# Kernel optimization log

Hardware: AMD Instinct MI355X
Metric: run time of the kernel (lower is better)

## Reference

```python
import jax, jax.numpy as jnp
import numpy as np

B, D, G, F, A = 262144, 128, 8, 80, 18  # batch, obs dim, n_games, n_features, max_actions


def setup_inputs() -> dict:
    key = jax.random.key(0)
    ks = jax.random.split(key, 10)
    s1 = 1.0 / np.sqrt(D)
    s2 = 1.0 / np.sqrt(F)
    state = jax.random.normal(ks[0], (B, D), dtype=jnp.float32)
    idx = jnp.sort(jax.random.randint(ks[1], (B,), 0, G, dtype=jnp.int32))
    W1 = jax.random.normal(ks[2], (G, F, D), dtype=jnp.float32) * s1
    b1 = jax.random.normal(ks[3], (G, F), dtype=jnp.float32) * s1
    W2 = jax.random.normal(ks[4], (F, F), dtype=jnp.float32) * s2
    b2 = jax.random.normal(ks[5], (F,), dtype=jnp.float32) * s2
    W3 = jax.random.normal(ks[6], (F, F), dtype=jnp.float32) * s2
    b3 = jax.random.normal(ks[7], (F,), dtype=jnp.float32) * s2
    W4 = jax.random.normal(ks[8], (G, A, F), dtype=jnp.float32) * s2
    b4 = jax.random.normal(ks[9], (G, A), dtype=jnp.float32) * s2
    return {"state": state, "idx": idx, "W1": W1, "b1": b1, "W2": W2, "b2": b2,
            "W3": W3, "b3": b3, "W4": W4, "b4": b4}


def reference(state, idx, W1, b1, W2, b2, W3, b3, W4, b4):
    state = state.astype(jnp.float32)
    n_games = W1.shape[0]
    # Routed first layer: each sample goes through its game's Linear(D->F).
    # Loop is over the small fixed set of games; batch dim stays vectorized.
    h1 = jnp.zeros((state.shape[0], W1.shape[1]), dtype=state.dtype)
    for g in range(n_games):
        hg = state @ W1[g].T + b1[g]  # [B, F]
        h1 = h1 + jnp.where((idx == g)[:, None], hg, jnp.zeros((), state.dtype))
    h1 = jax.nn.relu(h1)
    # Shared MLP (features == 'relu')
    h = jax.nn.relu(h1 @ W2.T + b2)
    h = jax.nn.relu(h @ W3.T + b3)
    # All per-game heads, stacked: q[b, g, a]
    q = jnp.einsum('bf,gaf->bga', h, W4) + b4  # [B, G, A]
    # Gather the head matching each sample's game (action=None branch)
    q_idx = jnp.take_along_axis(q, idx[:, None, None].astype(jnp.int32), axis=1)  # [B,1,A]
    return jnp.squeeze(q_idx, axis=1)  # [B, A]
```

## Files before the change

kernel.cpp:

```cpp
#include <hip/hip_runtime.h>


#define B_TOT   262144
#define DDIM    128
#define FDIM    80
#define ADIM    18
#define SH      104
#define THREADS 512
#define SLAB    128
#define NSLAB   4
#define GRID    (B_TOT / (SLAB * NSLAB))

#define W1SW    0
#define W2SW    81920
#define W3SW    89600
#define W4SW    97280
#define WTOT    121856

#define LW1     0
#define LW2     10240
#define LW3     17920
#define LHB     25600
#define LDS_SH  38912

typedef __attribute__((ext_vector_type(8))) short short8;
typedef __attribute__((ext_vector_type(4))) short short4v;
typedef __attribute__((ext_vector_type(2))) unsigned int uint2v;
typedef __attribute__((ext_vector_type(4))) float floatx4;
typedef __attribute__((ext_vector_type(2))) float floatx2;

static __device__ __forceinline__ unsigned short f2bf(float f) {
  union { float f; unsigned u; } v; v.f = f;
  unsigned r = v.u + 0x7fffu + ((v.u >> 16) & 1u);
  return (unsigned short)(r >> 16);
}
static __device__ __forceinline__ unsigned pk2(float a, float b) {
  union { float f; unsigned u; } x, y; x.f = a; y.f = b;
  unsigned ra = x.u + 0x7fffu + ((x.u >> 16) & 1u);
  unsigned rb = y.u + 0x7fffu + ((y.u >> 16) & 1u);
  return (ra >> 16) | (rb & 0xffff0000u);
}

__global__ void convert_weights(const float* __restrict__ W1, const float* __restrict__ W2,
                                const float* __restrict__ W3, const float* __restrict__ W4,
                                const float* __restrict__ b2, const float* __restrict__ b3,
                                const float* __restrict__ b4, unsigned short* __restrict__ ws) {
  int t = blockIdx.x * 256 + threadIdx.x;
  if (t >= WTOT) return;
  int chunk = t >> 9, r = t & 511;
  int lane = r >> 3, j = r & 7;
  int l16 = lane & 15, quad = lane >> 4;
  float val;
  if (chunk < 160) {
    int g = chunk / 20, rem = chunk % 20, ks = rem / 5, ct = rem % 5;
    int n = ct * 16 + l16, k = ks * 32 + quad * 8 + j;
    val = W1[(g * FDIM + n) * DDIM + k];
  } else if (chunk < 175) {
    int c = chunk - 160, ks = c / 5, ct = c % 5;
    int n = ct * 16 + l16, k = ks * 32 + quad * 8 + j;
    val = (k < FDIM) ? W2[n * FDIM + k] : (k == FDIM ? b2[n] : 0.f);
  } else if (chunk < 190) {
    int c = chunk - 175, ks = c / 5, ct = c % 5;
    int n = ct * 16 + l16, k = ks * 32 + quad * 8 + j;
    val = (k < FDIM) ? W3[n * FDIM + k] : (k == FDIM ? b3[n] : 0.f);
  } else {
    int c = chunk - 190, g = c / 6, rem = c % 6, ks = rem >> 1, ct = rem & 1;
    int n = ct * 16 + l16, k = ks * 32 + quad * 8 + j;
    val = (n < ADIM) ? ((k < FDIM) ? W4[(g * ADIM + n) * FDIM + k]
                                   : (k == FDIM ? b4[g * ADIM + n] : 0.f)) : 0.f;
  }
  ws[t] = f2bf(val);
}

static __device__ __forceinline__ void stage_game(
    int g, const unsigned short* __restrict__ wsw, unsigned short* smem,
    const float* __restrict__ b1, int tid, int quad, floatx4 b1v[5])
{
  __syncthreads();
  const short8* src = (const short8*)(wsw + W1SW + g * (20 * 512));
  short8* dst = (short8*)(smem + LW1);
#pragma unroll
  for (int i = 0; i < 3; ++i) {
    int t = i * THREADS + tid;
    if (t < 1280) dst[t] = src[t];
  }
  __syncthreads();
#pragma unroll
  for (int ct = 0; ct < 5; ++ct)
    b1v[ct] = *(const floatx4*)(b1 + g * FDIM + ct * 16 + quad * 4);
}

__global__ __launch_bounds__(THREADS, 4) void gym_fused(
    const float* __restrict__ state, const int* __restrict__ idx,
    const unsigned short* __restrict__ wsw, const float* __restrict__ b1,
    float* __restrict__ out)
{
  __shared__ __align__(16) unsigned short smem[LDS_SH];

  const int tid  = threadIdx.x;
  const int lane = tid & 63;
  const int wv   = tid >> 6;
  const int l16  = lane & 15;
  const int quad = lane >> 4;
  unsigned short* hbuf = smem + LHB + wv * (16 * SH);
  const size_t blk0 = (size_t)blockIdx.x * (SLAB * NSLAB);

  {
    const short8* src = (const short8*)(wsw + W2SW);
    short8* dst = (short8*)(smem + LW2);
#pragma unroll
    for (int i = 0; i < 4; ++i) {
      int t = i * THREADS + tid;
      if (t < 1920) dst[t] = src[t];
    }
  }
  {
    int row = lane >> 2, grp = lane & 3;
    short4v v = {0, 0, 0, 0};
    if (grp == 0) v[0] = (short)0x3F80;
    *(short4v*)(hbuf + row * SH + 80 + grp * 4) = v;
  }

  int curr_g = idx[blk0];
  floatx4 b1v[5];
  stage_game(curr_g, wsw, smem, b1, tid, quad, b1v);

  for (int it = 0; it < NSLAB; ++it) {
    const size_t slab0 = blk0 + (size_t)it * SLAB;
    const size_t trow  = slab0 + wv * 16;
    const int tg_lo = idx[slab0];
    const int tg_hi = idx[slab0 + SLAB - 1];
    const int midx  = idx[trow + l16];

    short8 afrag[4];
    {
      const float* sp = state + (trow + l16) * DDIM + quad * 8;
#pragma unroll
      for (int ks = 0; ks < 4; ++ks) {
        floatx4 va = *(const floatx4*)(sp + ks * 32);
        floatx4 vb = *(const floatx4*)(sp + ks * 32 + 4);
        short8 f;
        unsigned u0 = pk2(va[0], va[1]), u1 = pk2(va[2], va[3]);
        unsigned u2 = pk2(vb[0], vb[1]), u3 = pk2(vb[2], vb[3]);
        f[0] = (short)(u0 & 0xffff); f[1] = (short)(u0 >> 16);
        f[2] = (short)(u1 & 0xffff); f[3] = (short)(u1 >> 16);
        f[4] = (short)(u2 & 0xffff); f[5] = (short)(u2 >> 16);
        f[6] = (short)(u3 & 0xffff); f[7] = (short)(u3 >> 16);
        afrag[ks] = f;
      }
    }

    for (int g = tg_lo; g <= tg_hi; ++g) {
      if (g != curr_g) { stage_game(g, wsw, smem, b1, tid, quad, b1v); curr_g = g; }

      {
        floatx4 acc[5];
#pragma unroll
        for (int ct = 0; ct < 5; ++ct) acc[ct] = (floatx4){0.f, 0.f, 0.f, 0.f};
#pragma unroll
        for (int ks = 0; ks < 4; ++ks)
#pragma unroll
          for (int ct = 0; ct < 5; ++ct) {
            short8 wf = *(const short8*)(smem + LW1 + (ks * 5 + ct) * 512 + lane * 8);
            acc[ct] = __builtin_amdgcn_mfma_f32_16x16x32_bf16(wf, afrag[ks], acc[ct], 0, 0, 0);
          }
#pragma unroll
        for (int ct = 0; ct < 5; ++ct) {
          floatx4 v = acc[ct] + b1v[ct];
          uint2v u;
          u[0] = pk2(fmaxf(v[0], 0.f), fmaxf(v[1], 0.f));
          u[1] = pk2(fmaxf(v[2], 0.f), fmaxf(v[3], 0.f));
          if (midx == g)
            *(uint2v*)(hbuf + l16 * SH + ct * 16 + quad * 4) = u;
        }
      }
#pragma unroll
      for (int L = 0; L < 2; ++L) {
        short8 hf[3];
#pragma unroll
        for (int ks = 0; ks < 3; ++ks)
          hf[ks] = *(const short8*)(hbuf + l16 * SH + ks * 32 + quad * 8);
        floatx4 acc[5];
#pragma unroll
        for (int ct = 0; ct < 5; ++ct) acc[ct] = (floatx4){0.f, 0.f, 0.f, 0.f};
        const int lw = (L == 0) ? LW2 : LW3;
#pragma unroll
        for (int ks = 0; ks < 3; ++ks)
#pragma unroll
          for (int ct = 0; ct < 5; ++ct) {
            short8 wf = *(const short8*)(smem + lw + (ks * 5 + ct) * 512 + lane * 8);
            acc[ct] = __builtin_amdgcn_mfma_f32_16x16x32_bf16(wf, hf[ks], acc[ct], 0, 0, 0);
          }
#pragma unroll
        for (int ct = 0; ct < 5; ++ct) {
          uint2v u;
          u[0] = pk2(fmaxf(acc[ct][0], 0.f), fmaxf(acc[ct][1], 0.f));
          u[1] = pk2(fmaxf(acc[ct][2], 0.f), fmaxf(acc[ct][3], 0.f));
          *(uint2v*)(hbuf + l16 * SH + ct * 16 + quad * 4) = u;
        }
      }
      {
        short8 hf[3];
#pragma unroll
        for (int ks = 0; ks < 3; ++ks)
          hf[ks] = *(const short8*)(hbuf + l16 * SH + ks * 32 + quad * 8);
        floatx4 acc[2];
#pragma unroll
        for (int ct = 0; ct < 2; ++ct) acc[ct] = (floatx4){0.f, 0.f, 0.f, 0.f};
#pragma unroll
        for (int ks = 0; ks < 3; ++ks)
#pragma unroll
          for (int ct = 0; ct < 2; ++ct) {
            short8 wf = *(const short8*)(wsw + W4SW + (g * 6 + ks * 2 + ct) * 512 + lane * 8);
            acc[ct] = __builtin_amdgcn_mfma_f32_16x16x32_bf16(wf, hf[ks], acc[ct], 0, 0, 0);
          }
        if (midx == g) {
          float* op = out + (trow + l16) * ADIM;
          *(floatx2*)(op + quad * 4)     = (floatx2){acc[0][0], acc[0][1]};
          *(floatx2*)(op + quad * 4 + 2) = (floatx2){acc[0][2], acc[0][3]};
          if (quad == 0)
            *(floatx2*)(op + 16) = (floatx2){acc[1][0], acc[1][1]};
        }
      }
    }
  }
}

extern "C" void kernel_launch(void* const* d_in, const int* in_sizes, int n_in,
                              void* d_out, int out_size, void* d_ws, size_t ws_size,
                              hipStream_t stream) {
  const float* state = (const float*)d_in[0];
  const int*   idx   = (const int*)d_in[1];
  const float* W1    = (const float*)d_in[2];
  const float* b1    = (const float*)d_in[3];
  const float* W2    = (const float*)d_in[4];
  const float* b2    = (const float*)d_in[5];
  const float* W3    = (const float*)d_in[6];
  const float* b3    = (const float*)d_in[7];
  const float* W4    = (const float*)d_in[8];
  const float* b4    = (const float*)d_in[9];
  float*       out   = (float*)d_out;
  unsigned short* wsw = (unsigned short*)d_ws;

  convert_weights<<<(WTOT + 255) / 256, 256, 0, stream>>>(W1, W2, W3, W4, b2, b3, b4, wsw);
  gym_fused<<<GRID, THREADS, 0, stream>>>(state, idx, wsw, b1, out);
}
```

Measured before the change: 219.1 us.

## Process two 16-row tiles per wave, fold b1 into W1 MFMA, read W2/W3 from global

Each wave now handles 32 rows as two 16-row tiles, so every W1 fragment read from LDS feeds two MFMAs. The b1 bias is folded into the packed W1 as an extra K-slice multiplied by a constant ones fragment, which removes the per-game bias load and vector add. W2/W3 are no longer staged in LDS and are read from global/L2 inside the loop. The per-wave hidden buffer doubles in size. The extra MFMA slice and the global weight reads may add cost, and register pressure rises.

Result: slower. 357.6 us (+63.2%).

```diff
diff --git a/kernel.cpp b/kernel.cpp
--- a/kernel.cpp
+++ b/kernel.cpp
@@ -7,24 +7,22 @@
 #define ADIM    18
 #define SH      104
 #define THREADS 512
-#define SLAB    128
-#define NSLAB   4
+#define SLAB    256
+#define NSLAB   2
 #define GRID    (B_TOT / (SLAB * NSLAB))
 
 #define W1SW    0
-#define W2SW    81920
-#define W3SW    89600
-#define W4SW    97280
-#define WTOT    121856
+#define W2SW    102400
+#define W3SW    110080
+#define W4SW    117760
+#define NCHUNK  278
+#define WTOT    (NCHUNK * 512)
 
 #define LW1     0
-#define LW2     10240
-#define LW3     17920
-#define LHB     25600
-#define LDS_SH  38912
+#define LHB     12800
+#define LDS_SH  39424
 
 typedef __attribute__((ext_vector_type(8))) short short8;
-typedef __attribute__((ext_vector_type(4))) short short4v;
 typedef __attribute__((ext_vector_type(2))) unsigned int uint2v;
 typedef __attribute__((ext_vector_type(4))) float floatx4;
 typedef __attribute__((ext_vector_type(2))) float floatx2;
@@ -41,30 +39,32 @@
   return (ra >> 16) | (rb & 0xffff0000u);
 }
 
-__global__ void convert_weights(const float* __restrict__ W1, const float* __restrict__ W2,
-                                const float* __restrict__ W3, const float* __restrict__ W4,
-                                const float* __restrict__ b2, const float* __restrict__ b3,
-                                const float* __restrict__ b4, unsigned short* __restrict__ ws) {
+__global__ void convert_weights(const float* __restrict__ W1, const float* __restrict__ b1,
+                                const float* __restrict__ W2, const float* __restrict__ W3,
+                                const float* __restrict__ W4, const float* __restrict__ b2,
+                                const float* __restrict__ b3, const float* __restrict__ b4,
+                                unsigned short* __restrict__ ws) {
   int t = blockIdx.x * 256 + threadIdx.x;
   if (t >= WTOT) return;
   int chunk = t >> 9, r = t & 511;
   int lane = r >> 3, j = r & 7;
   int l16 = lane & 15, quad = lane >> 4;
   float val;
-  if (chunk < 160) {
-    int g = chunk / 20, rem = chunk % 20, ks = rem / 5, ct = rem % 5;
-    int n = ct * 16 + l16, k = ks * 32 + quad * 8 + j;
-    val = W1[(g * FDIM + n) * DDIM + k];
-  } else if (chunk < 175) {
-    int c = chunk - 160, ks = c / 5, ct = c % 5;
+  if (chunk < 200) {
+    int g = chunk / 25, rem = chunk % 25, ks = rem / 5, ct = rem % 5;
+    int n = ct * 16 + l16, k = ks * 32 + quad * 8 + j;
+    val = (ks < 4) ? W1[(g * FDIM + n) * DDIM + k]
+                   : ((quad == 0 && j == 0) ? b1[g * FDIM + n] : 0.f);
+  } else if (chunk < 215) {
+    int c = chunk - 200, ks = c / 5, ct = c % 5;
     int n = ct * 16 + l16, k = ks * 32 + quad * 8 + j;
     val = (k < FDIM) ? W2[n * FDIM + k] : (k == FDIM ? b2[n] : 0.f);
-  } else if (chunk < 190) {
-    int c = chunk - 175, ks = c / 5, ct = c % 5;
+  } else if (chunk < 230) {
+    int c = chunk - 215, ks = c / 5, ct = c % 5;
     int n = ct * 16 + l16, k = ks * 32 + quad * 8 + j;
     val = (k < FDIM) ? W3[n * FDIM + k] : (k == FDIM ? b3[n] : 0.f);
   } else {
-    int c = chunk - 190, g = c / 6, rem = c % 6, ks = rem >> 1, ct = rem & 1;
+    int c = chunk - 230, g = c / 6, rem = c % 6, ks = rem >> 1, ct = rem & 1;
     int n = ct * 16 + l16, k = ks * 32 + quad * 8 + j;
     val = (n < ADIM) ? ((k < FDIM) ? W4[(g * ADIM + n) * FDIM + k]
                                    : (k == FDIM ? b4[g * ADIM + n] : 0.f)) : 0.f;
@@ -73,27 +73,22 @@
 }
 
 static __device__ __forceinline__ void stage_game(
-    int g, const unsigned short* __restrict__ wsw, unsigned short* smem,
-    const float* __restrict__ b1, int tid, int quad, floatx4 b1v[5])
+    int g, const unsigned short* __restrict__ wsw, unsigned short* smem, int tid)
 {
   __syncthreads();
-  const short8* src = (const short8*)(wsw + W1SW + g * (20 * 512));
+  const short8* src = (const short8*)(wsw + W1SW + g * (25 * 512));
   short8* dst = (short8*)(smem + LW1);
 #pragma unroll
-  for (int i = 0; i < 3; ++i) {
+  for (int i = 0; i < 4; ++i) {
     int t = i * THREADS + tid;
-    if (t < 1280) dst[t] = src[t];
+    if (t < 1600) dst[t] = src[t];
   }
   __syncthreads();
-#pragma unroll
-  for (int ct = 0; ct < 5; ++ct)
-    b1v[ct] = *(const floatx4*)(b1 + g * FDIM + ct * 16 + quad * 4);
 }
 
 __global__ __launch_bounds__(THREADS, 4) void gym_fused(
     const float* __restrict__ state, const int* __restrict__ idx,
-    const unsigned short* __restrict__ wsw, const float* __restrict__ b1,
-    float* __restrict__ out)
+    const unsigned short* __restrict__ wsw, float* __restrict__ out)
 {
   __shared__ __align__(16) unsigned short smem[LDS_SH];
 
@@ -102,39 +97,34 @@
   const int wv   = tid >> 6;
   const int l16  = lane & 15;
   const int quad = lane >> 4;
-  unsigned short* hbuf = smem + LHB + wv * (16 * SH);
+  unsigned short* hbuf = smem + LHB + wv * (32 * SH);
   const size_t blk0 = (size_t)blockIdx.x * (SLAB * NSLAB);
 
   {
-    const short8* src = (const short8*)(wsw + W2SW);
-    short8* dst = (short8*)(smem + LW2);
-#pragma unroll
-    for (int i = 0; i < 4; ++i) {
-      int t = i * THREADS + tid;
-      if (t < 1920) dst[t] = src[t];
-    }
-  }
-  {
-    int row = lane >> 2, grp = lane & 3;
-    short4v v = {0, 0, 0, 0};
+    int row = lane >> 1, grp = lane & 1;
+    short8 v = (short8){0, 0, 0, 0, 0, 0, 0, 0};
     if (grp == 0) v[0] = (short)0x3F80;
-    *(short4v*)(hbuf + row * SH + 80 + grp * 4) = v;
-  }
+    *(short8*)(hbuf + row * SH + 80 + grp * 8) = v;
+  }
+
+  short8 bfrag = (short8){0, 0, 0, 0, 0, 0, 0, 0};
+  if (quad == 0) bfrag[0] = (short)0x3F80;
 
   int curr_g = idx[blk0];
-  floatx4 b1v[5];
-  stage_game(curr_g, wsw, smem, b1, tid, quad, b1v);
+  stage_game(curr_g, wsw, smem, tid);
 
   for (int it = 0; it < NSLAB; ++it) {
     const size_t slab0 = blk0 + (size_t)it * SLAB;
-    const size_t trow  = slab0 + wv * 16;
+    const size_t trow  = slab0 + wv * 32;
     const int tg_lo = idx[slab0];
     const int tg_hi = idx[slab0 + SLAB - 1];
-    const int midx  = idx[trow + l16];
-
-    short8 afrag[4];
-    {
-      const float* sp = state + (trow + l16) * DDIM + quad * 8;
+    const int midxA = idx[trow + l16];
+    const int midxB = idx[trow + 16 + l16];
+
+    short8 afrag[2][4];
+#pragma unroll
+    for (int t = 0; t < 2; ++t) {
+      const float* sp = state + (trow + t * 16 + l16) * DDIM + quad * 8;
 #pragma unroll
       for (int ks = 0; ks < 4; ++ks) {
         floatx4 va = *(const floatx4*)(sp + ks * 32);
@@ -146,80 +136,97 @@
         f[2] = (short)(u1 & 0xffff); f[3] = (short)(u1 >> 16);
         f[4] = (short)(u2 & 0xffff); f[5] = (short)(u2 >> 16);
         f[6] = (short)(u3 & 0xffff); f[7] = (short)(u3 >> 16);
-        afrag[ks] = f;
+        afrag[t][ks] = f;
       }
     }
 
     for (int g = tg_lo; g <= tg_hi; ++g) {
-      if (g != curr_g) { stage_game(g, wsw, smem, b1, tid, quad, b1v); curr_g = g; }
+      if (g != curr_g) { stage_game(g, wsw, smem, tid); curr_g = g; }
 
       {
-        floatx4 acc[5];
-#pragma unroll
-        for (int ct = 0; ct < 5; ++ct) acc[ct] = (floatx4){0.f, 0.f, 0.f, 0.f};
-#pragma unroll
-        for (int ks = 0; ks < 4; ++ks)
+        floatx4 accA[5], accB[5];
+#pragma unroll
+        for (int ct = 0; ct < 5; ++ct) {
+          accA[ct] = (floatx4){0.f, 0.f, 0.f, 0.f};
+          accB[ct] = (floatx4){0.f, 0.f, 0.f, 0.f};
+        }
+#pragma unroll
+        for (int ks = 0; ks < 5; ++ks) {
+          short8 bA = (ks < 4) ? afrag[0][ks] : bfrag;
+          short8 bB = (ks < 4) ? afrag[1][ks] : bfrag;
 #pragma unroll
           for (int ct = 0; ct < 5; ++ct) {
             short8 wf = *(const short8*)(smem + LW1 + (ks * 5 + ct) * 512 + lane * 8);
-            acc[ct] = __builtin_amdgcn_mfma_f32_16x16x32_bf16(wf, afrag[ks], acc[ct], 0, 0, 0);
+            accA[ct] = __builtin_amdgcn_mfma_f32_16x16x32_bf16(wf, bA, accA[ct], 0, 0, 0);
+            accB[ct] = __builtin_amdgcn_mfma_f32_16x16x32_bf16(wf, bB, accB[ct], 0, 0, 0);
           }
+        }
 #pragma unroll
         for (int ct = 0; ct < 5; ++ct) {
-          floatx4 v = acc[ct] + b1v[ct];
-          uint2v u;
-          u[0] = pk2(fmaxf(v[0], 0.f), fmaxf(v[1], 0.f));
-          u[1] = pk2(fmaxf(v[2], 0.f), fmaxf(v[3], 0.f));
-          if (midx == g)
-            *(uint2v*)(hbuf + l16 * SH + ct * 16 + quad * 4) = u;
+          uint2v uA, uB;
+          uA[0] = pk2(fmaxf(accA[ct][0], 0.f), fmaxf(accA[ct][1], 0.f));
+          uA[1] = pk2(fmaxf(accA[ct][2], 0.f), fmaxf(accA[ct][3], 0.f));
+          uB[0] = pk2(fmaxf(accB[ct][0], 0.f), fmaxf(accB[ct][1], 0.f));
+          uB[1] = pk2(fmaxf(accB[ct][2], 0.f), fmaxf(accB[ct][3], 0.f));
+          if (midxA == g)
+            *(uint2v*)(hbuf + l16 * SH + ct * 16 + quad * 4) = uA;
+          if (midxB == g)
+            *(uint2v*)(hbuf + (16 + l16) * SH + ct * 16 + quad * 4) = uB;
         }
       }
-#pragma unroll
-      for (int L = 0; L < 2; ++L) {
-        short8 hf[3];
-#pragma unroll
-        for (int ks = 0; ks < 3; ++ks)
-          hf[ks] = *(const short8*)(hbuf + l16 * SH + ks * 32 + quad * 8);
-        floatx4 acc[5];
-#pragma unroll
-        for (int ct = 0; ct < 5; ++ct) acc[ct] = (floatx4){0.f, 0.f, 0.f, 0.f};
-        const int lw = (L == 0) ? LW2 : LW3;
-#pragma unroll
-        for (int ks = 0; ks < 3; ++ks)
+
+#pragma unroll
+      for (int t = 0; t < 2; ++t) {
+        unsigned short* hrow = hbuf + (t * 16 + l16) * SH;
+        const int midx = (t == 0) ? midxA : midxB;
+
+#pragma unroll
+        for (int L = 0; L < 2; ++L) {
+          short8 hf[3];
+#pragma unroll
+          for (int ks = 0; ks < 3; ++ks)
+            hf[ks] = *(const short8*)(hrow + ks * 32 + quad * 8);
+          floatx4 acc[5];
+#pragma unroll
+          for (int ct = 0; ct < 5; ++ct) acc[ct] = (floatx4){0.f, 0.f, 0.f, 0.f};
+          const unsigned short* wbase = wsw + ((L == 0) ? W2SW : W3SW);
+#pragma unroll
+          for (int ks = 0; ks < 3; ++ks)
+#pragma unroll
+            for (int ct = 0; ct < 5; ++ct) {
+              short8 wf = *(const short8*)(wbase + (ks * 5 + ct) * 512 + lane * 8);
+              acc[ct] = __builtin_amdgcn_mfma_f32_16x16x32_bf16(wf, hf[ks], acc[ct], 0, 0, 0);
+            }
 #pragma unroll
           for (int ct = 0; ct < 5; ++ct) {
-            short8 wf = *(const short8*)(smem + lw + (ks * 5 + ct) * 512 + lane * 8);
-            acc[ct] = __builtin_amdgcn_mfma_f32_16x16x32_bf16(wf, hf[ks], acc[ct], 0, 0, 0);
+            uint2v u;
+            u[0] = pk2(fmaxf(acc[ct][0], 0.f), fmaxf(acc[ct][1], 0.f));
+            u[1] = pk2(fmaxf(acc[ct][2], 0.f), fmaxf(acc[ct][3], 0.f));
+            *(uint2v*)(hrow + ct * 16 + quad * 4) = u;
           }
-#pragma unroll
-        for (int ct = 0; ct < 5; ++ct) {
-          uint2v u;
-          u[0] = pk2(fmaxf(acc[ct][0], 0.f), fmaxf(acc[ct][1], 0.f));
-          u[1] = pk2(fmaxf(acc[ct][2], 0.f), fmaxf(acc[ct][3], 0.f));
-          *(uint2v*)(hbuf + l16 * SH + ct * 16 + quad * 4) = u;
-        }
-      }
-      {
-        short8 hf[3];
-#pragma unroll
-        for (int ks = 0; ks < 3; ++ks)
-          hf[ks] = *(const short8*)(hbuf + l16 * SH + ks * 32 + quad * 8);
-        floatx4 acc[2];
-#pragma unroll
-        for (int ct = 0; ct < 2; ++ct) acc[ct] = (floatx4){0.f, 0.f, 0.f, 0.f};
-#pragma unroll
-        for (int ks = 0; ks < 3; ++ks)
-#pragma unroll
-          for (int ct = 0; ct < 2; ++ct) {
-            short8 wf = *(const short8*)(wsw + W4SW + (g * 6 + ks * 2 + ct) * 512 + lane * 8);
-            acc[ct] = __builtin_amdgcn_mfma_f32_16x16x32_bf16(wf, hf[ks], acc[ct], 0, 0, 0);
+        }
+        {
+          short8 hf[3];
+#pragma unroll
+          for (int ks = 0; ks < 3; ++ks)
+            hf[ks] = *(const short8*)(hrow + ks * 32 + quad * 8);
+          floatx4 acc[2];
+#pragma unroll
+          for (int ct = 0; ct < 2; ++ct) acc[ct] = (floatx4){0.f, 0.f, 0.f, 0.f};
+#pragma unroll
+          for (int ks = 0; ks < 3; ++ks)
+#pragma unroll
+            for (int ct = 0; ct < 2; ++ct) {
+              short8 wf = *(const short8*)(wsw + W4SW + (g * 6 + ks * 2 + ct) * 512 + lane * 8);
+              acc[ct] = __builtin_amdgcn_mfma_f32_16x16x32_bf16(wf, hf[ks], acc[ct], 0, 0, 0);
+            }
+          if (midx == g) {
+            float* op = out + (trow + t * 16 + l16) * ADIM;
+            *(floatx2*)(op + quad * 4)     = (floatx2){acc[0][0], acc[0][1]};
+            *(floatx2*)(op + quad * 4 + 2) = (floatx2){acc[0][2], acc[0][3]};
+            if (quad == 0)
+              *(floatx2*)(op + 16) = (floatx2){acc[1][0], acc[1][1]};
           }
-        if (midx == g) {
-          float* op = out + (trow + l16) * ADIM;
-          *(floatx2*)(op + quad * 4)     = (floatx2){acc[0][0], acc[0][1]};
-          *(floatx2*)(op + quad * 4 + 2) = (floatx2){acc[0][2], acc[0][3]};
-          if (quad == 0)
-            *(floatx2*)(op + 16) = (floatx2){acc[1][0], acc[1][1]};
         }
       }
     }
@@ -242,6 +249,6 @@
   float*       out   = (float*)d_out;
   unsigned short* wsw = (unsigned short*)d_ws;
 
-  convert_weights<<<(WTOT + 255) / 256, 256, 0, stream>>>(W1, W2, W3, W4, b2, b3, b4, wsw);
-  gym_fused<<<GRID, THREADS, 0, stream>>>(state, idx, wsw, b1, out);
-}
+  convert_weights<<<(WTOT + 255) / 256, 256, 0, stream>>>(W1, b1, W2, W3, W4, b2, b3, b4, wsw);
+  gym_fused<<<GRID, THREADS, 0, stream>>>(state, idx, wsw, out);
+}
```
